# Kernel tuning notes

Hardware: AMD Instinct MI355X
Metric: run time of the kernel (lower is better)

The kernel has to match this reference:

```python
import jax, jax.numpy as jnp
import numpy as np

T, B, N = 2048, 32, 1024   # time, batch, dan_hidden_size
H = 8                      # multihead_size
N2 = 128                   # attention_hidden_size
K = N // H                 # N_H = 128 per-head dim
K2 = N2 // H               # N2_H = 16 per-head attention dim


def setup_inputs() -> dict:
    key = jax.random.key(0)
    ks = jax.random.split(key, 10)
    s_n = 1.0 / np.sqrt(N)
    s_k = 1.0 / np.sqrt(K)
    s_k2 = 1.0 / np.sqrt(K2)
    return {
        "hyp": jax.random.normal(ks[0], (T, B, N), dtype=jnp.float32),
        # H independent per-head linears N -> K, stacked: (H, K, N)
        "Wmh": jax.random.uniform(ks[1], (H, K, N), minval=-s_n, maxval=s_n, dtype=jnp.float32),
        "bmh": jax.random.uniform(ks[2], (H, K), minval=-s_n, maxval=s_n, dtype=jnp.float32),
        # shared W: K -> K2
        "W": jax.random.uniform(ks[3], (K2, K), minval=-s_k, maxval=s_k, dtype=jnp.float32),
        "bW": jax.random.uniform(ks[4], (K2,), minval=-s_k, maxval=s_k, dtype=jnp.float32),
        # shared W_m: K -> K2
        "Wm": jax.random.uniform(ks[5], (K2, K), minval=-s_k, maxval=s_k, dtype=jnp.float32),
        "bWm": jax.random.uniform(ks[6], (K2,), minval=-s_k, maxval=s_k, dtype=jnp.float32),
        # shared W_h: K2 -> 1
        "Wh": jax.random.uniform(ks[7], (K2,), minval=-s_k2, maxval=s_k2, dtype=jnp.float32),
        "bWh": jax.random.uniform(ks[8], (), minval=-s_k2, maxval=s_k2, dtype=jnp.float32),
        "dan_hidden_size": N,
        "attention_hidden_size": N2,
        "multihead_size": H,
    }


def reference(hyp, Wmh, bmh, W, bW, Wm, bWm, Wh, bWh,
              dan_hidden_size, attention_hidden_size, multihead_size):
    # Per-head projections, all heads at once: (B, T, H, K)
    X = jnp.einsum('tbn,hkn->bthk', hyp, Wmh) + bmh
    # mean over time (original x.mean(0)): (B, H, K)
    m = X.mean(axis=1)
    # tanh-gated additive scoring: (B, T, H, K2)
    g = jnp.tanh(jnp.einsum('bthk,qk->bthq', X, W) + bW) \
        * jnp.tanh(jnp.einsum('bhk,qk->bhq', m, Wm) + bWm)[:, None]
    # scalar score per (b, t, h), softmax over time
    s = jnp.einsum('bthq,q->bth', g, Wh) + bWh
    a = jax.nn.softmax(s, axis=1)                       # (B, T, H)
    # attention-weighted sum over time: (B, H, K)
    c = jnp.einsum('bth,bthk->bhk', a, X)
    # concat heads along feature dim (head-major order, matches torch.cat)
    Bsz = c.shape[0]
    return c.reshape(Bsz, -1)                            # (B, N)
```

## Files before the change

kernel.cpp:

```cpp
#include <hip/hip_runtime.h>
#include <hip/hip_bf16.h>

#define T_DIM 2048
#define B_DIM 32
#define N_DIM 1024
#define H_DIM 8
#define K_DIM 128
#define Q_DIM 16

typedef __bf16 bf16x8 __attribute__((ext_vector_type(8)));
typedef __bf16 bf16x4 __attribute__((ext_vector_type(4)));
typedef float  f32x4  __attribute__((ext_vector_type(4)));

__device__ inline bf16x8 cvt8(float4 a, float4 b) {
    bf16x8 r;
    r[0] = (__bf16)a.x; r[1] = (__bf16)a.y; r[2] = (__bf16)a.z; r[3] = (__bf16)a.w;
    r[4] = (__bf16)b.x; r[5] = (__bf16)b.y; r[6] = (__bf16)b.z; r[7] = (__bf16)b.w;
    return r;
}

__global__ __launch_bounds__(256)
void cvt_f32_bf16(const float* __restrict__ s, __bf16* __restrict__ d)
{
    const long i = ((long)blockIdx.x * 256 + threadIdx.x) * 8;
    float4 a = *(const float4*)(s + i);
    float4 b = *(const float4*)(s + i + 4);
    *(bf16x8*)(d + i) = cvt8(a, b);
}

__global__ __launch_bounds__(512, 1)
void gemm_x_8ph(const __bf16* __restrict__ A, const __bf16* __restrict__ Bw,
                const float* __restrict__ bias, __bf16* __restrict__ X,
                float* __restrict__ mpart)
{
    __shared__ __bf16 ldsA[2][16384];
    __shared__ __bf16 ldsB[2][16384];

    const int tid  = threadIdx.x;
    const int lane = tid & 63;
    const int w    = tid >> 6;
    const int wm   = w >> 2;
    const int wn   = w & 3;

    const int bid  = blockIdx.x;
    const int wgid = (bid & 7) * 128 + (bid >> 3);
    const int bm   = wgid >> 2;
    const int bn   = wgid & 3;
    const long row0 = (long)bm * 256;
    const long col0 = (long)bn * 256;

    const int srow = w * 8 + (lane >> 3);
    const int scol = ((lane & 7) ^ (lane >> 3)) * 8;
    const __bf16* Ag = A  + (row0 + srow) * 1024 + scol;
    const __bf16* Bg = Bw + (col0 + srow) * 1024 + scol;
    const int ldst = w * 512;

    const int fr = lane & 15;
    const int g2 = lane >> 4;
    const int x7 = lane & 7;

    const __bf16* aK0 = &ldsA[0][(wm * 128 + fr) * 64] + ((g2    ) ^ x7) * 8;
    const __bf16* aK1 = &ldsA[0][(wm * 128 + fr) * 64] + ((4 + g2) ^ x7) * 8;
    const __bf16* bK0 = &ldsB[0][(wn * 64  + fr) * 64] + ((g2    ) ^ x7) * 8;
    const __bf16* bK1 = &ldsB[0][(wn * 64  + fr) * 64] + ((4 + g2) ^ x7) * 8;

    f32x4 acc[8][4];
    #pragma unroll
    for (int i = 0; i < 8; ++i)
        #pragma unroll
        for (int j = 0; j < 4; ++j)
            acc[i][j] = f32x4{0.f, 0.f, 0.f, 0.f};

    #pragma unroll
    for (int j = 0; j < 4; ++j) {
        __builtin_amdgcn_global_load_lds(
            (const __attribute__((address_space(1))) void*)(Ag + (long)j * 65536),
            (__attribute__((address_space(3))) void*)(&ldsA[0][j * 4096 + ldst]), 16, 0, 0);
        __builtin_amdgcn_global_load_lds(
            (const __attribute__((address_space(1))) void*)(Bg + (long)j * 65536),
            (__attribute__((address_space(3))) void*)(&ldsB[0][j * 4096 + ldst]), 16, 0, 0);
    }
    #pragma unroll
    for (int j = 0; j < 4; ++j) {
        __builtin_amdgcn_global_load_lds(
            (const __attribute__((address_space(1))) void*)(Ag + (long)j * 65536 + 64),
            (__attribute__((address_space(3))) void*)(&ldsA[1][j * 4096 + ldst]), 16, 0, 0);
        __builtin_amdgcn_global_load_lds(
            (const __attribute__((address_space(1))) void*)(Bg + (long)j * 65536 + 64),
            (__attribute__((address_space(3))) void*)(&ldsB[1][j * 4096 + ldst]), 16, 0, 0);
    }
    asm volatile("s_waitcnt vmcnt(8)" ::: "memory");
    __builtin_amdgcn_sched_barrier(0);
    __builtin_amdgcn_s_barrier();

    bf16x8 a0[4], b0[4];
    #pragma unroll
    for (int mi = 0; mi < 4; ++mi) a0[mi] = *(const bf16x8*)(aK0 + mi * 1024);
    #pragma unroll
    for (int ni = 0; ni < 4; ++ni) b0[ni] = *(const bf16x8*)(bK0 + ni * 1024);

    const __bf16* AgN = Ag + 128;
    const __bf16* BgN = Bg + 128;

    #define KTBODY(SO_, SN_, STG_, VM_, LAST_)                                 \
    {                                                                          \
        bf16x8 a0h[4], b1[4], a1[4], a1h[4];                                   \
        _Pragma("unroll") for (int mi = 0; mi < 4; ++mi)                       \
            a0h[mi] = *(const bf16x8*)(aK1 + (SO_) + mi * 1024);               \
        _Pragma("unroll") for (int ni = 0; ni < 4; ++ni)                       \
            b1[ni]  = *(const bf16x8*)(bK1 + (SO_) + ni * 1024);               \
        __builtin_amdgcn_s_setprio(1);                                         \
        _Pragma("unroll") for (int mi = 0; mi < 4; ++mi)                       \
            _Pragma("unroll") for (int ni = 0; ni < 4; ++ni)                   \
                acc[mi][ni] = __builtin_amdgcn_mfma_f32_16x16x32_bf16(         \
                    b0[ni], a0[mi], acc[mi][ni], 0, 0, 0);                     \
        __builtin_amdgcn_s_setprio(0);                                         \
        _Pragma("unroll") for (int mi = 0; mi < 4; ++mi) {                     \
            a1[mi]  = *(const bf16x8*)(aK0 + (SO_) + (mi + 4) * 1024);         \
            a1h[mi] = *(const bf16x8*)(aK1 + (SO_) + (mi + 4) * 1024);         \
        }                                                                      \
        __builtin_amdgcn_s_setprio(1);                                         \
        _Pragma("unroll") for (int mi = 0; mi < 4; ++mi)                       \
            _Pragma("unroll") for (int ni = 0; ni < 4; ++ni)                   \
                acc[mi][ni] = __builtin_amdgcn_mfma_f32_16x16x32_bf16(         \
                    b1[ni], a0h[mi], acc[mi][ni], 0, 0, 0);                    \
        __builtin_amdgcn_s_setprio(0);                                         \
        asm volatile("s_waitcnt lgkmcnt(0)" ::: "memory");                     \
        __builtin_amdgcn_sched_barrier(0);                                     \
        __builtin_amdgcn_s_barrier();                                          \
        if (STG_) {                                                            \
            _Pragma("unroll") for (int j = 0; j < 4; ++j)                      \
                __builtin_amdgcn_global_load_lds(                              \
                    (const __attribute__((address_space(1))) void*)(AgN + (long)j * 65536 + ((STG_) == 2 ? 64 : 0)), \
                    (__attribute__((address_space(3))) void*)(&ldsA[(SO_) ? 1 : 0][j * 4096 + ldst]), 16, 0, 0); \
            _Pragma("unroll") for (int j = 0; j < 4; ++j)                      \
                __builtin_amdgcn_global_load_lds(                              \
                    (const __attribute__((address_space(1))) void*)(BgN + (long)j * 65536 + ((STG_) == 2 ? 64 : 0)), \
                    (__attribute__((address_space(3))) void*)(&ldsB[(SO_) ? 1 : 0][j * 4096 + ldst]), 16, 0, 0); \
        }                                                                      \
        __builtin_amdgcn_s_setprio(1);                                         \
        _Pragma("unroll") for (int mi = 0; mi < 4; ++mi)                       \
            _Pragma("unroll") for (int ni = 0; ni < 4; ++ni)                   \
                acc[mi + 4][ni] = __builtin_amdgcn_mfma_f32_16x16x32_bf16(     \
                    b0[ni], a1[mi], acc[mi + 4][ni], 0, 0, 0);                 \
        __builtin_amdgcn_s_setprio(0);                                         \
        if ((VM_) == 8) { asm volatile("s_waitcnt vmcnt(8)" ::: "memory"); }   \
        else if ((VM_) == 0) { asm volatile("s_waitcnt vmcnt(0)" ::: "memory"); } \
        __builtin_amdgcn_sched_barrier(0);                                     \
        if (!(LAST_)) {                                                        \
            __builtin_amdgcn_s_barrier();                                      \
            _Pragma("unroll") for (int mi = 0; mi < 4; ++mi)                   \
                a0[mi] = *(const bf16x8*)(aK0 + (SN_) + mi * 1024);            \
            _Pragma("unroll") for (int ni = 0; ni < 4; ++ni)                   \
                b0[ni] = *(const bf16x8*)(bK0 + (SN_) + ni * 1024);            \
        }                                                                      \
        __builtin_amdgcn_s_setprio(1);                                         \
        _Pragma("unroll") for (int mi = 0; mi < 4; ++mi)                       \
            _Pragma("unroll") for (int ni = 0; ni < 4; ++ni)                   \
                acc[mi + 4][ni] = __builtin_amdgcn_mfma_f32_16x16x32_bf16(     \
                    b1[ni], a1h[mi], acc[mi + 4][ni], 0, 0, 0);                \
        __builtin_amdgcn_s_setprio(0);                                         \
    }

    #pragma unroll 1
    for (int ii = 0; ii < 7; ++ii) {
        KTBODY(0,     16384, 1, 8, 0);
        KTBODY(16384, 0,     2, 8, 0);
        AgN += 128; BgN += 128;
    }
    KTBODY(0,     16384, 0, 0, 0);
    KTBODY(16384, 0,     0, -1, 1);
    #undef KTBODY

    const int g4 = lane >> 4;
    const long colb = col0 + wn * 64 + g4 * 4;

    float4 bias4[4];
    #pragma unroll
    for (int ni = 0; ni < 4; ++ni)
        bias4[ni] = *(const float4*)(bias + colb + ni * 16);

    f32x4 msum[2][4];
    #pragma unroll
    for (int bh = 0; bh < 2; ++bh)
        #pragma unroll
        for (int ni = 0; ni < 4; ++ni)
            msum[bh][ni] = f32x4{0.f, 0.f, 0.f, 0.f};

    #pragma unroll
    for (int mi = 0; mi < 8; ++mi) {
        const long row = row0 + wm * 128 + mi * 16 + fr;
        #pragma unroll
        for (int ni = 0; ni < 4; ++ni) {
            f32x4 xv;
            xv[0] = acc[mi][ni][0] + bias4[ni].x;
            xv[1] = acc[mi][ni][1] + bias4[ni].y;
            xv[2] = acc[mi][ni][2] + bias4[ni].z;
            xv[3] = acc[mi][ni][3] + bias4[ni].w;
            bf16x4 xb;
            xb[0] = (__bf16)xv[0]; xb[1] = (__bf16)xv[1];
            xb[2] = (__bf16)xv[2]; xb[3] = (__bf16)xv[3];
            *(bf16x4*)(X + row * 1024 + colb + ni * 16) = xb;
            msum[mi & 1][ni] += xv;
        }
    }

    float* ldsf = (float*)&ldsA[0][0];
    __syncthreads();
    if (wm == 1) {
        #pragma unroll
        for (int bh = 0; bh < 2; ++bh)
            #pragma unroll
            for (int ni = 0; ni < 4; ++ni)
                *(f32x4*)(ldsf + (bh * 16 + fr) * 256 + wn * 64 + ni * 16 + g4 * 4) = msum[bh][ni];
    }
    __syncthreads();
    if (wm == 0) {
        #pragma unroll
        for (int bh = 0; bh < 2; ++bh) {
            const int b = bh * 16 + fr;
            #pragma unroll
            for (int ni = 0; ni < 4; ++ni) {
                f32x4 other = *(const f32x4*)(ldsf + b * 256 + wn * 64 + ni * 16 + g4 * 4);
                f32x4 tot = msum[bh][ni] + other;
                *(f32x4*)(mpart + ((long)bm * 32 + b) * 1024 + colb + ni * 16) = tot;
            }
        }
    }
}

__global__ __launch_bounds__(256)
void gate2_k(const float* __restrict__ mpart, const float* __restrict__ Wm,
             const float* __restrict__ bWm, float* __restrict__ g2)
{
    __shared__ float mrow[1024];
    const int b = blockIdx.x;
    const int j4 = threadIdx.x * 4;
    f32x4 s = f32x4{0.f, 0.f, 0.f, 0.f};
    for (int bm = 0; bm < 256; ++bm)
        s += *(const f32x4*)(mpart + ((long)bm * 32 + b) * 1024 + j4);
    mrow[j4 + 0] = s[0] * (1.0f / 2048.0f);
    mrow[j4 + 1] = s[1] * (1.0f / 2048.0f);
    mrow[j4 + 2] = s[2] * (1.0f / 2048.0f);
    mrow[j4 + 3] = s[3] * (1.0f / 2048.0f);
    __syncthreads();
    if (threadIdx.x < 128) {
        const int h = threadIdx.x >> 4;
        const int q = threadIdx.x & 15;
        float d = bWm[q];
        #pragma unroll 8
        for (int k = 0; k < 128; ++k) d += mrow[h * 128 + k] * Wm[q * 128 + k];
        g2[(b * 8 + h) * 16 + q] = tanhf(d);
    }
}

__global__ __launch_bounds__(256)
void scores_k(const __bf16* __restrict__ X, const float* __restrict__ W,
              const float* __restrict__ bW, const float* __restrict__ g2,
              const float* __restrict__ Wh, const float* __restrict__ bWh,
              float* __restrict__ sbuf)
{
    const int tid   = threadIdx.x;
    const int lane  = tid & 63;
    const int w     = tid >> 6;
    const int gw    = blockIdx.x * 4 + w;
    const int rbase = gw * 16;
    const int q     = lane & 15;
    const int g4    = lane >> 4;

    bf16x8 bfr[4];
    #pragma unroll
    for (int c = 0; c < 4; ++c) {
        const float* wp = W + q * 128 + c * 32 + g4 * 8;
        float4 w0 = *(const float4*)wp;
        float4 w1 = *(const float4*)(wp + 4);
        bfr[c] = cvt8(w0, w1);
    }
    const __bf16* xp = X + (long)(rbase + q) * 128 + g4 * 8;
    bf16x8 afr[4];
    #pragma unroll
    for (int c = 0; c < 4; ++c) afr[c] = *(const bf16x8*)(xp + c * 32);

    f32x4 acc = f32x4{0.f, 0.f, 0.f, 0.f};
    #pragma unroll
    for (int c = 0; c < 4; ++c)
        acc = __builtin_amdgcn_mfma_f32_16x16x32_bf16(afr[c], bfr[c], acc, 0, 0, 0);

    const float whq  = Wh[q];
    const float bWv  = bW[q];
    const float bWhv = *bWh;
    #pragma unroll
    for (int r = 0; r < 4; ++r) {
        const int row = rbase + g4 * 4 + r;
        const int h   = row & 7;
        const int bt  = row >> 3;
        const int b   = bt & 31;
        const int t   = bt >> 5;
        float val = tanhf(acc[r] + bWv) * g2[(b * 8 + h) * 16 + q] * whq;
        val += __shfl_xor(val, 1);
        val += __shfl_xor(val, 2);
        val += __shfl_xor(val, 4);
        val += __shfl_xor(val, 8);
        if (q == 0) sbuf[(b * 8 + h) * 2048 + t] = val + bWhv;
    }
}

__global__ __launch_bounds__(256)
void softmax_k(float* __restrict__ s)
{
    __shared__ float red[256];
    const int bh = blockIdx.x;
    const int tid = threadIdx.x;
    float* row = s + bh * 2048;
    float4 v0 = *(const float4*)(row + tid * 8);
    float4 v1 = *(const float4*)(row + tid * 8 + 4);
    float v[8] = {v0.x, v0.y, v0.z, v0.w, v1.x, v1.y, v1.z, v1.w};
    float mx = v[0];
    #pragma unroll
    for (int i = 1; i < 8; ++i) mx = fmaxf(mx, v[i]);
    red[tid] = mx;
    __syncthreads();
    for (int st = 128; st > 0; st >>= 1) {
        if (tid < st) red[tid] = fmaxf(red[tid], red[tid + st]);
        __syncthreads();
    }
    mx = red[0];
    __syncthreads();
    float sum = 0.f;
    #pragma unroll
    for (int i = 0; i < 8; ++i) { v[i] = expf(v[i] - mx); sum += v[i]; }
    red[tid] = sum;
    __syncthreads();
    for (int st = 128; st > 0; st >>= 1) {
        if (tid < st) red[tid] += red[tid + st];
        __syncthreads();
    }
    const float inv = 1.0f / red[0];
    *(float4*)(row + tid * 8)     = make_float4(v[0] * inv, v[1] * inv, v[2] * inv, v[3] * inv);
    *(float4*)(row + tid * 8 + 4) = make_float4(v[4] * inv, v[5] * inv, v[6] * inv, v[7] * inv);
}

__global__ __launch_bounds__(256)
void wsum_k(const float* __restrict__ a, const __bf16* __restrict__ X,
            float* __restrict__ wpart)
{
    __shared__ float pk[8 * 128];
    const int bx = blockIdx.x;
    const int tc = bx & 7;
    const int bh = bx >> 3;
    const int b  = bh >> 3;
    const int h  = bh & 7;
    const int tid = threadIdx.x;
    const int kq = tid & 31;
    const int tr = tid >> 5;
    const float* ar = a + bh * 2048 + tc * 256;
    float a0 = 0.f, a1 = 0.f, a2 = 0.f, a3 = 0.f;
    #pragma unroll 4
    for (int i = tr; i < 256; i += 8) {
        const int t = tc * 256 + i;
        const float av = ar[i];
        bf16x4 xv = *(const bf16x4*)(X + (long)(t * 32 + b) * 1024 + h * 128 + kq * 4);
        a0 += av * (float)xv[0];
        a1 += av * (float)xv[1];
        a2 += av * (float)xv[2];
        a3 += av * (float)xv[3];
    }
    pk[tr * 128 + kq * 4 + 0] = a0;
    pk[tr * 128 + kq * 4 + 1] = a1;
    pk[tr * 128 + kq * 4 + 2] = a2;
    pk[tr * 128 + kq * 4 + 3] = a3;
    __syncthreads();
    if (tid < 128) {
        float s2 = 0.f;
        #pragma unroll
        for (int r = 0; r < 8; ++r) s2 += pk[r * 128 + tid];
        wpart[(long)bx * 128 + tid] = s2;
    }
}

__global__ __launch_bounds__(256)
void wsum_fin(const float* __restrict__ wpart, float* __restrict__ out)
{
    const int idx = blockIdx.x * 256 + threadIdx.x;
    const int k  = idx & 127;
    const int bh = idx >> 7;
    const int b  = bh >> 3;
    const int h  = bh & 7;
    float s = 0.f;
    #pragma unroll
    for (int tc = 0; tc < 8; ++tc) s += wpart[(bh * 8 + tc) * 128 + k];
    out[b * 1024 + h * 128 + k] = s;
}

extern "C" void kernel_launch(void* const* d_in, const int* in_sizes, int n_in,
                              void* d_out, int out_size, void* d_ws, size_t ws_size,
                              hipStream_t stream)
{
    const float* hyp = (const float*)d_in[0];
    const float* Wmh = (const float*)d_in[1];
    const float* bmh = (const float*)d_in[2];
    const float* W   = (const float*)d_in[3];
    const float* bW  = (const float*)d_in[4];
    const float* Wm  = (const float*)d_in[5];
    const float* bWm = (const float*)d_in[6];
    const float* Wh  = (const float*)d_in[7];
    const float* bWh = (const float*)d_in[8];
    float* out = (float*)d_out;

    char* ws = (char*)d_ws;
    const size_t SZ_X   = 134217728;
    const size_t SZ_AB  = 134217728;
    const size_t SZ_BB  = 2097152;
    const size_t SZ_MP  = 33554432;
    const size_t SZ_G2  = 16384;
    const size_t SZ_SB  = 2097152;

    size_t off = 0;
    __bf16* X     = (__bf16*)(ws + off); off += SZ_X;
    __bf16* Ab    = (__bf16*)(ws + off); off += SZ_AB;
    __bf16* Bb    = (__bf16*)(ws + off); off += SZ_BB;
    float*  mpart = (float*) (ws + off); off += SZ_MP;
    float*  g2    = (float*) (ws + off); off += SZ_G2;
    float*  sbuf  = (float*) (ws + off); off += SZ_SB;
    float*  wpart = (float*) (ws + off);

    cvt_f32_bf16<<<32768, 256, 0, stream>>>(hyp, Ab);
    cvt_f32_bf16<<<512,   256, 0, stream>>>(Wmh, Bb);
    gemm_x_8ph<<<1024, 512, 0, stream>>>(Ab, Bb, bmh, X, mpart);
    gate2_k<<<32, 256, 0, stream>>>(mpart, Wm, bWm, g2);
    scores_k<<<8192, 256, 0, stream>>>(X, W, bW, g2, Wh, bWh, sbuf);
    softmax_k<<<256, 256, 0, stream>>>(sbuf);
    wsum_k<<<2048, 256, 0, stream>>>(sbuf, X, wpart);
    wsum_fin<<<128, 256, 0, stream>>>(wpart, out);
}
```

Measured before the change: 341.9 us.

## Restructure GEMM K-loop into four-phase ping-pong with finer-grained LDS staging

Rewrites the main loop of the bf16 projection GEMM into four MFMA phases per K-tile. Each phase loads its fragments from LDS, issues a half-tile of global-to-LDS prefetch, and synchronizes with barriers around the MFMA block. The A and B prefetches are staggered so the next A tile is streamed while B stays one stage behind, and vmcnt waits are relaxed to 4. The intent is to interleave memory traffic more evenly with matrix math, at the cost of many more workgroup barriers and lgkmcnt(0) waits per tile.

```diff
diff --git a/kernel.cpp b/kernel.cpp
--- a/kernel.cpp
+++ b/kernel.cpp
@@ -35,6 +35,8 @@
 {
     __shared__ __bf16 ldsA[2][16384];
     __shared__ __bf16 ldsB[2][16384];
+    __bf16* ldsAf = &ldsA[0][0];
+    __bf16* ldsBf = &ldsB[0][0];
 
     const int tid  = threadIdx.x;
     const int lane = tid & 63;
@@ -59,10 +61,10 @@
     const int g2 = lane >> 4;
     const int x7 = lane & 7;
 
-    const __bf16* aK0 = &ldsA[0][(wm * 128 + fr) * 64] + ((g2    ) ^ x7) * 8;
-    const __bf16* aK1 = &ldsA[0][(wm * 128 + fr) * 64] + ((4 + g2) ^ x7) * 8;
-    const __bf16* bK0 = &ldsB[0][(wn * 64  + fr) * 64] + ((g2    ) ^ x7) * 8;
-    const __bf16* bK1 = &ldsB[0][(wn * 64  + fr) * 64] + ((4 + g2) ^ x7) * 8;
+    const __bf16* aK0 = ldsAf + (wm * 128 + fr) * 64 + ((g2    ) ^ x7) * 8;
+    const __bf16* aK1 = ldsAf + (wm * 128 + fr) * 64 + ((4 + g2) ^ x7) * 8;
+    const __bf16* bK0 = ldsBf + (wn * 64  + fr) * 64 + ((g2    ) ^ x7) * 8;
+    const __bf16* bK1 = ldsBf + (wn * 64  + fr) * 64 + ((4 + g2) ^ x7) * 8;
 
     f32x4 acc[8][4];
     #pragma unroll
@@ -71,106 +73,113 @@
         for (int j = 0; j < 4; ++j)
             acc[i][j] = f32x4{0.f, 0.f, 0.f, 0.f};
 
-    #pragma unroll
-    for (int j = 0; j < 4; ++j) {
-        __builtin_amdgcn_global_load_lds(
-            (const __attribute__((address_space(1))) void*)(Ag + (long)j * 65536),
-            (__attribute__((address_space(3))) void*)(&ldsA[0][j * 4096 + ldst]), 16, 0, 0);
-        __builtin_amdgcn_global_load_lds(
-            (const __attribute__((address_space(1))) void*)(Bg + (long)j * 65536),
-            (__attribute__((address_space(3))) void*)(&ldsB[0][j * 4096 + ldst]), 16, 0, 0);
-    }
-    #pragma unroll
-    for (int j = 0; j < 4; ++j) {
-        __builtin_amdgcn_global_load_lds(
-            (const __attribute__((address_space(1))) void*)(Ag + (long)j * 65536 + 64),
-            (__attribute__((address_space(3))) void*)(&ldsA[1][j * 4096 + ldst]), 16, 0, 0);
-        __builtin_amdgcn_global_load_lds(
-            (const __attribute__((address_space(1))) void*)(Bg + (long)j * 65536 + 64),
-            (__attribute__((address_space(3))) void*)(&ldsB[1][j * 4096 + ldst]), 16, 0, 0);
-    }
-    asm volatile("s_waitcnt vmcnt(8)" ::: "memory");
+    #define GLDA(SRC_, DST_) __builtin_amdgcn_global_load_lds( \
+        (const __attribute__((address_space(1))) void*)(SRC_), \
+        (__attribute__((address_space(3))) void*)(DST_), 16, 0, 0)
+
+    #pragma unroll
+    for (int j = 0; j < 2; ++j) GLDA(Ag + (long)j * 65536,          ldsAf + j * 4096 + ldst);
+    #pragma unroll
+    for (int j = 0; j < 2; ++j) GLDA(Ag + 131072 + (long)j * 65536, ldsAf + 8192 + j * 4096 + ldst);
+    #pragma unroll
+    for (int j = 0; j < 2; ++j) GLDA(Bg + (long)j * 65536,          ldsBf + j * 4096 + ldst);
+    #pragma unroll
+    for (int j = 0; j < 2; ++j) GLDA(Bg + 131072 + (long)j * 65536, ldsBf + 8192 + j * 4096 + ldst);
+    #pragma unroll
+    for (int j = 0; j < 2; ++j) GLDA(Bg + 64 + (long)j * 65536,          ldsBf + 16384 + j * 4096 + ldst);
+    #pragma unroll
+    for (int j = 0; j < 2; ++j) GLDA(Bg + 64 + 131072 + (long)j * 65536, ldsBf + 16384 + 8192 + j * 4096 + ldst);
+    asm volatile("s_waitcnt vmcnt(4)" ::: "memory");
     __builtin_amdgcn_sched_barrier(0);
     __builtin_amdgcn_s_barrier();
 
-    bf16x8 a0[4], b0[4];
-    #pragma unroll
-    for (int mi = 0; mi < 4; ++mi) a0[mi] = *(const bf16x8*)(aK0 + mi * 1024);
-    #pragma unroll
-    for (int ni = 0; ni < 4; ++ni) b0[ni] = *(const bf16x8*)(bK0 + ni * 1024);
-
-    const __bf16* AgN = Ag + 128;
+    const __bf16* AgN = Ag + 64;
     const __bf16* BgN = Bg + 128;
 
-    #define KTBODY(SO_, SN_, STG_, VM_, LAST_)                                 \
+    #define MFMA16(AF_, BF_, OFF_)                                             \
+        __builtin_amdgcn_s_setprio(1);                                         \
+        _Pragma("unroll") for (int mi = 0; mi < 4; ++mi)                       \
+            _Pragma("unroll") for (int ni = 0; ni < 4; ++ni)                   \
+                acc[mi + (OFF_)][ni] = __builtin_amdgcn_mfma_f32_16x16x32_bf16(\
+                    BF_[ni], AF_[mi], acc[mi + (OFF_)][ni], 0, 0, 0);          \
+        __builtin_amdgcn_s_setprio(0);
+
+    #define LGKM0()                                                            \
+        asm volatile("s_waitcnt lgkmcnt(0)" ::: "memory");                     \
+        __builtin_amdgcn_sched_barrier(0);
+
+    #define KTBODY(SO_, SN_, KO_, STGA_, STGB_, VM_)                           \
     {                                                                          \
-        bf16x8 a0h[4], b1[4], a1[4], a1h[4];                                   \
+        bf16x8 a0[4], b0[4], a0h[4], b1[4], a1[4], a1h[4];                     \
+                   \
+        _Pragma("unroll") for (int mi = 0; mi < 4; ++mi)                       \
+            a0[mi] = *(const bf16x8*)(aK0 + (SO_) + mi * 1024);                \
+        _Pragma("unroll") for (int ni = 0; ni < 4; ++ni)                       \
+            b0[ni] = *(const bf16x8*)(bK0 + (SO_) + ni * 1024);                \
+        if (STGA_) {                                                           \
+            _Pragma("unroll") for (int j = 0; j < 2; ++j)                      \
+                GLDA(AgN + (KO_) + (long)j * 65536,                            \
+                     ldsAf + (SN_) + j * 4096 + ldst);                         \
+        }                                                                      \
+        __builtin_amdgcn_s_barrier();                                          \
+        LGKM0();                                                               \
+        MFMA16(a0, b0, 0);                                                     \
+        __builtin_amdgcn_s_barrier();                                          \
+                  \
         _Pragma("unroll") for (int mi = 0; mi < 4; ++mi)                       \
             a0h[mi] = *(const bf16x8*)(aK1 + (SO_) + mi * 1024);               \
         _Pragma("unroll") for (int ni = 0; ni < 4; ++ni)                       \
             b1[ni]  = *(const bf16x8*)(bK1 + (SO_) + ni * 1024);               \
-        __builtin_amdgcn_s_setprio(1);                                         \
+        if (STGA_) {                                                           \
+            _Pragma("unroll") for (int j = 0; j < 2; ++j)                      \
+                GLDA(AgN + (KO_) + 131072 + (long)j * 65536,                   \
+                     ldsAf + (SN_) + 8192 + j * 4096 + ldst);                  \
+        }                                                                      \
+        __builtin_amdgcn_s_barrier();                                          \
+        LGKM0();                                                               \
+        MFMA16(a0h, b1, 0);                                                    \
+        __builtin_amdgcn_s_barrier();                                          \
+                    \
         _Pragma("unroll") for (int mi = 0; mi < 4; ++mi)                       \
-            _Pragma("unroll") for (int ni = 0; ni < 4; ++ni)                   \
-                acc[mi][ni] = __builtin_amdgcn_mfma_f32_16x16x32_bf16(         \
-                    b0[ni], a0[mi], acc[mi][ni], 0, 0, 0);                     \
-        __builtin_amdgcn_s_setprio(0);                                         \
-        _Pragma("unroll") for (int mi = 0; mi < 4; ++mi) {                     \
-            a1[mi]  = *(const bf16x8*)(aK0 + (SO_) + (mi + 4) * 1024);         \
+            a1[mi] = *(const bf16x8*)(aK0 + (SO_) + (mi + 4) * 1024);          \
+        if (STGB_) {                                                           \
+            _Pragma("unroll") for (int j = 0; j < 2; ++j)                      \
+                GLDA(BgN + (KO_) + (long)j * 65536,                            \
+                     ldsBf + (SO_) + j * 4096 + ldst);                         \
+        }                                                                      \
+        __builtin_amdgcn_s_barrier();                                          \
+        LGKM0();                                                               \
+        MFMA16(a1, b0, 4);                                                     \
+        __builtin_amdgcn_s_barrier();                                          \
+                 \
+        _Pragma("unroll") for (int mi = 0; mi < 4; ++mi)                       \
             a1h[mi] = *(const bf16x8*)(aK1 + (SO_) + (mi + 4) * 1024);         \
+        if (STGB_) {                                                           \
+            _Pragma("unroll") for (int j = 0; j < 2; ++j)                      \
+                GLDA(BgN + (KO_) + 131072 + (long)j * 65536,                   \
+                     ldsBf + (SO_) + 8192 + j * 4096 + ldst);                  \
         }                                                                      \
-        __builtin_amdgcn_s_setprio(1);                                         \
-        _Pragma("unroll") for (int mi = 0; mi < 4; ++mi)                       \
-            _Pragma("unroll") for (int ni = 0; ni < 4; ++ni)                   \
-                acc[mi][ni] = __builtin_amdgcn_mfma_f32_16x16x32_bf16(         \
-                    b1[ni], a0h[mi], acc[mi][ni], 0, 0, 0);                    \
-        __builtin_amdgcn_s_setprio(0);                                         \
-        asm volatile("s_waitcnt lgkmcnt(0)" ::: "memory");                     \
-        __builtin_amdgcn_sched_barrier(0);                                     \
-        __builtin_amdgcn_s_barrier();                                          \
-        if (STG_) {                                                            \
-            _Pragma("unroll") for (int j = 0; j < 4; ++j)                      \
-                __builtin_amdgcn_global_load_lds(                              \
-                    (const __attribute__((address_space(1))) void*)(AgN + (long)j * 65536 + ((STG_) == 2 ? 64 : 0)), \
-                    (__attribute__((address_space(3))) void*)(&ldsA[(SO_) ? 1 : 0][j * 4096 + ldst]), 16, 0, 0); \
-            _Pragma("unroll") for (int j = 0; j < 4; ++j)                      \
-                __builtin_amdgcn_global_load_lds(                              \
-                    (const __attribute__((address_space(1))) void*)(BgN + (long)j * 65536 + ((STG_) == 2 ? 64 : 0)), \
-                    (__attribute__((address_space(3))) void*)(&ldsB[(SO_) ? 1 : 0][j * 4096 + ldst]), 16, 0, 0); \
-        }                                                                      \
-        __builtin_amdgcn_s_setprio(1);                                         \
-        _Pragma("unroll") for (int mi = 0; mi < 4; ++mi)                       \
-            _Pragma("unroll") for (int ni = 0; ni < 4; ++ni)                   \
-                acc[mi + 4][ni] = __builtin_amdgcn_mfma_f32_16x16x32_bf16(     \
-                    b0[ni], a1[mi], acc[mi + 4][ni], 0, 0, 0);                 \
-        __builtin_amdgcn_s_setprio(0);                                         \
-        if ((VM_) == 8) { asm volatile("s_waitcnt vmcnt(8)" ::: "memory"); }   \
+        if ((VM_) == 4)      { asm volatile("s_waitcnt vmcnt(4)" ::: "memory"); } \
         else if ((VM_) == 0) { asm volatile("s_waitcnt vmcnt(0)" ::: "memory"); } \
         __builtin_amdgcn_sched_barrier(0);                                     \
-        if (!(LAST_)) {                                                        \
-            __builtin_amdgcn_s_barrier();                                      \
-            _Pragma("unroll") for (int mi = 0; mi < 4; ++mi)                   \
-                a0[mi] = *(const bf16x8*)(aK0 + (SN_) + mi * 1024);            \
-            _Pragma("unroll") for (int ni = 0; ni < 4; ++ni)                   \
-                b0[ni] = *(const bf16x8*)(bK0 + (SN_) + ni * 1024);            \
-        }                                                                      \
-        __builtin_amdgcn_s_setprio(1);                                         \
-        _Pragma("unroll") for (int mi = 0; mi < 4; ++mi)                       \
-            _Pragma("unroll") for (int ni = 0; ni < 4; ++ni)                   \
-                acc[mi + 4][ni] = __builtin_amdgcn_mfma_f32_16x16x32_bf16(     \
-                    b1[ni], a1h[mi], acc[mi + 4][ni], 0, 0, 0);                \
-        __builtin_amdgcn_s_setprio(0);                                         \
+        __builtin_amdgcn_s_barrier();                                          \
+        LGKM0();                                                               \
+        MFMA16(a1h, b1, 4);                                                    \
+        __builtin_amdgcn_s_barrier();                                          \
     }
 
     #pragma unroll 1
     for (int ii = 0; ii < 7; ++ii) {
-        KTBODY(0,     16384, 1, 8, 0);
-        KTBODY(16384, 0,     2, 8, 0);
+        KTBODY(0,     16384, 0,  1, 1, 4);
+        KTBODY(16384, 0,     64, 1, 1, 4);
         AgN += 128; BgN += 128;
     }
-    KTBODY(0,     16384, 0, 0, 0);
-    KTBODY(16384, 0,     0, -1, 1);
+    KTBODY(0,     16384, 0, 1, 0, 0);
+    KTBODY(16384, 0,     0, 0, 0, -1);
     #undef KTBODY
+    #undef MFMA16
+    #undef LGKM0
+    #undef GLDA
 
     const int g4 = lane >> 4;
     const long colb = col0 + wn * 64 + g4 * 4;
@@ -205,7 +214,7 @@
         }
     }
 
-    float* ldsf = (float*)&ldsA[0][0];
+    float* ldsf = (float*)ldsAf;
     __syncthreads();
     if (wm == 1) {
         #pragma unroll
```

Result: faster. 328.4 us (-3.9%).
